# Kernel tuning notes

Measured on AMD Instinct MI355X. Metric: run time of the kernel, lower is better.

## Reference

```python
import jax, jax.numpy as jnp
import numpy as np

SIGMA = 7.0
KERNEL_SIZE = int(2 * np.ceil(SIGMA * 2) + 1)  # 29
PAD = (KERNEL_SIZE - 1) // 2  # 14


def _gaussian_kernel2d():
    variance = SIGMA ** 2
    coords = jnp.arange(KERNEL_SIZE, dtype=jnp.float32)
    mean = (KERNEL_SIZE - 1) / 2.0
    xg, yg = jnp.meshgrid(coords, coords, indexing='xy')
    k = jnp.exp(-((xg - mean) ** 2 + (yg - mean) ** 2) / (2.0 * variance))
    k = k / (2.0 * np.pi * variance)
    return k / k.sum()  # [K, K]


def setup_inputs() -> dict:
    key = jax.random.key(0)
    x = jax.random.normal(key, (8, 64, 256, 256), dtype=jnp.float32)
    return {"x": x}


def reference(x):
    channels = x.shape[1]
    k2d = _gaussian_kernel2d().astype(x.dtype)
    # depthwise weights: [C, 1, K, K] (OIHW with feature_group_count=C)
    w = jnp.broadcast_to(k2d, (channels, 1, KERNEL_SIZE, KERNEL_SIZE))
    xp = jnp.pad(x, ((0, 0), (0, 0), (PAD, PAD), (PAD, PAD)), mode='reflect')
    out = jax.lax.conv_general_dilated(
        xp, w,
        window_strides=(1, 1),
        padding='VALID',
        dimension_numbers=('NCHW', 'OIHW', 'NCHW'),
        feature_group_count=channels,
    )
    return out
```

## Files before the change

kernel.cpp:

```cpp
#include <hip/hip_runtime.h>

#define IMG   256
#define SROWS 32
#define KS    29
#define PAD   14
#define LDSS  292
#define MOFF  16

static constexpr float GK[15] = {
    1.0f,        0.98984780f, 0.96000544f, 0.91225408f, 0.84936581f,
    0.77483743f, 0.69256933f, 0.60653066f, 0.52045012f, 0.43756474f,
    0.36044779f, 0.29092381f, 0.23006630f, 0.17826398f, 0.13533528f
};
static constexpr float GSUM =
    GK[0] + 2.0f * (GK[1] + GK[2] + GK[3] + GK[4] + GK[5] + GK[6] + GK[7] +
                    GK[8] + GK[9] + GK[10] + GK[11] + GK[12] + GK[13] + GK[14]);
static constexpr float WT[29] = {
    GK[14]/GSUM, GK[13]/GSUM, GK[12]/GSUM, GK[11]/GSUM, GK[10]/GSUM, GK[9]/GSUM, GK[8]/GSUM,
    GK[7]/GSUM,  GK[6]/GSUM,  GK[5]/GSUM,  GK[4]/GSUM,  GK[3]/GSUM,  GK[2]/GSUM, GK[1]/GSUM,
    GK[0]/GSUM,
    GK[1]/GSUM,  GK[2]/GSUM,  GK[3]/GSUM,  GK[4]/GSUM,  GK[5]/GSUM,  GK[6]/GSUM, GK[7]/GSUM,
    GK[8]/GSUM,  GK[9]/GSUM,  GK[10]/GSUM, GK[11]/GSUM, GK[12]/GSUM, GK[13]/GSUM, GK[14]/GSUM
};

__device__ __forceinline__ int refl(int p) {
    int a = p < 0 ? -p : p;
    int b = 2 * (IMG - 1) - a;
    return a < b ? a : b;
}

__global__ __launch_bounds__(256, 4)
void gauss_v6(const float* __restrict__ x, float* __restrict__ out) {
    __shared__ float s[SROWS * LDSS];

    const int t   = threadIdx.x;
    const int img = blockIdx.y;
    const int y0  = blockIdx.x * SROWS;

    const float* __restrict__ src = x   + (size_t)img * (IMG * IMG);
    float*       __restrict__ dst = out + (size_t)img * (IMG * IMG);

    const int cq = t & 63;
    const int rg = t >> 6;
    const int c0 = cq * 4;

    {
        const int brow = y0 + rg * 8 - PAD;

        float4 acc[8];
        #pragma unroll
        for (int j = 0; j < 8; ++j) acc[j] = make_float4(0.f, 0.f, 0.f, 0.f);

        const bool interior = (brow >= 0) && (brow + 35 < IMG);
        if (interior) {
            const float* p = src + (size_t)brow * IMG + c0;
            #pragma unroll
            for (int ch = 0; ch < 3; ++ch) {
                float4 v[12];
                #pragma unroll
                for (int i = 0; i < 12; ++i)
                    v[i] = *(const float4*)(p + (ch * 12 + i) * IMG);
                #pragma unroll
                for (int i = 0; i < 12; ++i) {
                    const int sdx = ch * 12 + i;
                    #pragma unroll
                    for (int j = 0; j < 8; ++j) {
                        const int k = sdx - j;
                        if (k >= 0 && k < KS) {
                            acc[j].x += WT[k] * v[i].x;
                            acc[j].y += WT[k] * v[i].y;
                            acc[j].z += WT[k] * v[i].z;
                            acc[j].w += WT[k] * v[i].w;
                        }
                    }
                }
            }
        } else {
            #pragma unroll
            for (int ch = 0; ch < 3; ++ch) {
                float4 v[12];
                #pragma unroll
                for (int i = 0; i < 12; ++i)
                    v[i] = *(const float4*)(src + (size_t)refl(brow + ch * 12 + i) * IMG + c0);
                #pragma unroll
                for (int i = 0; i < 12; ++i) {
                    const int sdx = ch * 12 + i;
                    #pragma unroll
                    for (int j = 0; j < 8; ++j) {
                        const int k = sdx - j;
                        if (k >= 0 && k < KS) {
                            acc[j].x += WT[k] * v[i].x;
                            acc[j].y += WT[k] * v[i].y;
                            acc[j].z += WT[k] * v[i].z;
                            acc[j].w += WT[k] * v[i].w;
                        }
                    }
                }
            }
        }

        #pragma unroll
        for (int j = 0; j < 8; ++j)
            *(float4*)&s[(rg * 8 + j) * LDSS + MOFF + c0] = acc[j];

        if (c0 <= PAD || c0 + 3 >= IMG - 1 - PAD) {
            #pragma unroll
            for (int q = 0; q < 4; ++q) {
                const int c = c0 + q;
                if (c >= 1 && c <= PAD) {
                    #pragma unroll
                    for (int j = 0; j < 8; ++j) {
                        const float v = q == 0 ? acc[j].x : q == 1 ? acc[j].y : q == 2 ? acc[j].z : acc[j].w;
                        s[(rg * 8 + j) * LDSS + (MOFF - c)] = v;
                    }
                } else if (c >= IMG - 1 - PAD && c <= IMG - 2) {
                    #pragma unroll
                    for (int j = 0; j < 8; ++j) {
                        const float v = q == 0 ? acc[j].x : q == 1 ? acc[j].y : q == 2 ? acc[j].z : acc[j].w;
                        s[(rg * 8 + j) * LDSS + (MOFF + 2 * (IMG - 1) - c)] = v;
                    }
                }
            }
        }
    }
    __syncthreads();

    {
        #pragma unroll
        for (int r = 0; r < 8; ++r) {
            const int row = rg * 8 + r;
            const float4* w = (const float4*)&s[row * LDSS + c0];
            float4 v[9];
            #pragma unroll
            for (int m = 0; m < 9; ++m) v[m] = w[m];

            float4 o = make_float4(0.f, 0.f, 0.f, 0.f);
            #pragma unroll
            for (int m = 0; m < 9; ++m) {
                #pragma unroll
                for (int q = 0; q < 4; ++q) {
                    const int p = 4 * m + q;
                    const float val = q == 0 ? v[m].x : q == 1 ? v[m].y : q == 2 ? v[m].z : v[m].w;
                    #pragma unroll
                    for (int c = 0; c < 4; ++c) {
                        const int k = p - c - 2;
                        if (k >= 0 && k < KS) {
                            if (c == 0) o.x += WT[k] * val;
                            else if (c == 1) o.y += WT[k] * val;
                            else if (c == 2) o.z += WT[k] * val;
                            else o.w += WT[k] * val;
                        }
                    }
                }
            }
            *(float4*)&dst[(size_t)(y0 + row) * IMG + c0] = o;
        }
    }
}

extern "C" void kernel_launch(void* const* d_in, const int* in_sizes, int n_in,
                              void* d_out, int out_size, void* d_ws, size_t ws_size,
                              hipStream_t stream) {
    const float* x = (const float*)d_in[0];
    float* out = (float*)d_out;
    const int images = in_sizes[0] / (IMG * IMG);
    dim3 grid(IMG / SROWS, images);
    gauss_v6<<<grid, dim3(256), 0, stream>>>(x, out);
}
```

Before: 96.76 us.

## Halve row tile and register-block the horizontal pass at 16 outputs per thread

Each block now covers 16 output rows instead of 32. The vertical pass gives each thread 4 rows instead of 8, and launch bounds now allow 8 blocks per CU instead of 4. The horizontal pass is rewritten so that each thread produces 16 consecutive outputs of one row from 48 LDS values, instead of 4 outputs from 36 values for each of 8 rows. This cuts LDS reads per output and raises occupancy. The cost is a larger vertical halo per output row, which means more redundant global or L2 reads, and more accumulators live per thread in the horizontal pass.

```diff
diff --git a/kernel.cpp b/kernel.cpp
--- a/kernel.cpp
+++ b/kernel.cpp
@@ -1,7 +1,7 @@
 #include <hip/hip_runtime.h>
 
 #define IMG   256
-#define SROWS 32
+#define SROWS 16
 #define KS    29
 #define PAD   14
 #define LDSS  292
@@ -29,8 +29,8 @@
     return a < b ? a : b;
 }
 
-__global__ __launch_bounds__(256, 4)
-void gauss_v6(const float* __restrict__ x, float* __restrict__ out) {
+__global__ __launch_bounds__(256, 8)
+void gauss_v7(const float* __restrict__ x, float* __restrict__ out) {
     __shared__ float s[SROWS * LDSS];
 
     const int t   = threadIdx.x;
@@ -40,31 +40,30 @@
     const float* __restrict__ src = x   + (size_t)img * (IMG * IMG);
     float*       __restrict__ dst = out + (size_t)img * (IMG * IMG);
 
-    const int cq = t & 63;
-    const int rg = t >> 6;
-    const int c0 = cq * 4;
+    {
+        const int cq   = t & 63;
+        const int rg   = t >> 6;
+        const int c0   = cq * 4;
+        const int brow = y0 + rg * 4 - PAD;
 
-    {
-        const int brow = y0 + rg * 8 - PAD;
+        float4 acc[4];
+        #pragma unroll
+        for (int j = 0; j < 4; ++j) acc[j] = make_float4(0.f, 0.f, 0.f, 0.f);
 
-        float4 acc[8];
-        #pragma unroll
-        for (int j = 0; j < 8; ++j) acc[j] = make_float4(0.f, 0.f, 0.f, 0.f);
-
-        const bool interior = (brow >= 0) && (brow + 35 < IMG);
+        const bool interior = (brow >= 0) && (brow + 31 < IMG);
         if (interior) {
             const float* p = src + (size_t)brow * IMG + c0;
             #pragma unroll
-            for (int ch = 0; ch < 3; ++ch) {
-                float4 v[12];
+            for (int ch = 0; ch < 4; ++ch) {
+                float4 v[8];
                 #pragma unroll
-                for (int i = 0; i < 12; ++i)
-                    v[i] = *(const float4*)(p + (ch * 12 + i) * IMG);
+                for (int i = 0; i < 8; ++i)
+                    v[i] = *(const float4*)(p + (ch * 8 + i) * IMG);
                 #pragma unroll
-                for (int i = 0; i < 12; ++i) {
-                    const int sdx = ch * 12 + i;
+                for (int i = 0; i < 8; ++i) {
+                    const int sdx = ch * 8 + i;
                     #pragma unroll
-                    for (int j = 0; j < 8; ++j) {
+                    for (int j = 0; j < 4; ++j) {
                         const int k = sdx - j;
                         if (k >= 0 && k < KS) {
                             acc[j].x += WT[k] * v[i].x;
@@ -77,16 +76,16 @@
             }
         } else {
             #pragma unroll
-            for (int ch = 0; ch < 3; ++ch) {
-                float4 v[12];
+            for (int ch = 0; ch < 4; ++ch) {
+                float4 v[8];
                 #pragma unroll
-                for (int i = 0; i < 12; ++i)
-                    v[i] = *(const float4*)(src + (size_t)refl(brow + ch * 12 + i) * IMG + c0);
+                for (int i = 0; i < 8; ++i)
+                    v[i] = *(const float4*)(src + (size_t)refl(brow + ch * 8 + i) * IMG + c0);
                 #pragma unroll
-                for (int i = 0; i < 12; ++i) {
-                    const int sdx = ch * 12 + i;
+                for (int i = 0; i < 8; ++i) {
+                    const int sdx = ch * 8 + i;
                     #pragma unroll
-                    for (int j = 0; j < 8; ++j) {
+                    for (int j = 0; j < 4; ++j) {
                         const int k = sdx - j;
                         if (k >= 0 && k < KS) {
                             acc[j].x += WT[k] * v[i].x;
@@ -100,8 +99,8 @@
         }
 
         #pragma unroll
-        for (int j = 0; j < 8; ++j)
-            *(float4*)&s[(rg * 8 + j) * LDSS + MOFF + c0] = acc[j];
+        for (int j = 0; j < 4; ++j)
+            *(float4*)&s[(rg * 4 + j) * LDSS + MOFF + c0] = acc[j];
 
         if (c0 <= PAD || c0 + 3 >= IMG - 1 - PAD) {
             #pragma unroll
@@ -109,15 +108,15 @@
                 const int c = c0 + q;
                 if (c >= 1 && c <= PAD) {
                     #pragma unroll
-                    for (int j = 0; j < 8; ++j) {
+                    for (int j = 0; j < 4; ++j) {
                         const float v = q == 0 ? acc[j].x : q == 1 ? acc[j].y : q == 2 ? acc[j].z : acc[j].w;
-                        s[(rg * 8 + j) * LDSS + (MOFF - c)] = v;
+                        s[(rg * 4 + j) * LDSS + (MOFF - c)] = v;
                     }
                 } else if (c >= IMG - 1 - PAD && c <= IMG - 2) {
                     #pragma unroll
-                    for (int j = 0; j < 8; ++j) {
+                    for (int j = 0; j < 4; ++j) {
                         const float v = q == 0 ? acc[j].x : q == 1 ? acc[j].y : q == 2 ? acc[j].z : acc[j].w;
-                        s[(rg * 8 + j) * LDSS + (MOFF + 2 * (IMG - 1) - c)] = v;
+                        s[(rg * 4 + j) * LDSS + (MOFF + 2 * (IMG - 1) - c)] = v;
                     }
                 }
             }
@@ -126,35 +125,39 @@
     __syncthreads();
 
     {
+        const int row = t >> 4;
+        const int cg  = t & 15;
+        const int c0b = cg * 16;
+
+        float acc[16];
         #pragma unroll
-        for (int r = 0; r < 8; ++r) {
-            const int row = rg * 8 + r;
-            const float4* w = (const float4*)&s[row * LDSS + c0];
-            float4 v[9];
+        for (int c = 0; c < 16; ++c) acc[c] = 0.f;
+
+        const float4* w = (const float4*)&s[row * LDSS + c0b];
+        #pragma unroll
+        for (int ch = 0; ch < 3; ++ch) {
+            float4 v[4];
             #pragma unroll
-            for (int m = 0; m < 9; ++m) v[m] = w[m];
-
-            float4 o = make_float4(0.f, 0.f, 0.f, 0.f);
+            for (int m = 0; m < 4; ++m) v[m] = w[ch * 4 + m];
             #pragma unroll
-            for (int m = 0; m < 9; ++m) {
+            for (int m = 0; m < 4; ++m) {
                 #pragma unroll
                 for (int q = 0; q < 4; ++q) {
-                    const int p = 4 * m + q;
+                    const int e = (ch * 4 + m) * 4 + q;
                     const float val = q == 0 ? v[m].x : q == 1 ? v[m].y : q == 2 ? v[m].z : v[m].w;
                     #pragma unroll
-                    for (int c = 0; c < 4; ++c) {
-                        const int k = p - c - 2;
-                        if (k >= 0 && k < KS) {
-                            if (c == 0) o.x += WT[k] * val;
-                            else if (c == 1) o.y += WT[k] * val;
-                            else if (c == 2) o.z += WT[k] * val;
-                            else o.w += WT[k] * val;
-                        }
+                    for (int c = 0; c < 16; ++c) {
+                        const int k = e - 2 - c;
+                        if (k >= 0 && k < KS) acc[c] += WT[k] * val;
                     }
                 }
             }
-            *(float4*)&dst[(size_t)(y0 + row) * IMG + c0] = o;
         }
+
+        float4* orow = (float4*)&dst[(size_t)(y0 + row) * IMG + c0b];
+        #pragma unroll
+        for (int m = 0; m < 4; ++m)
+            orow[m] = make_float4(acc[4*m+0], acc[4*m+1], acc[4*m+2], acc[4*m+3]);
     }
 }
 
@@ -165,5 +168,5 @@
     float* out = (float*)d_out;
     const int images = in_sizes[0] / (IMG * IMG);
     dim3 grid(IMG / SROWS, images);
-    gauss_v6<<<grid, dim3(256), 0, stream>>>(x, out);
+    gauss_v7<<<grid, dim3(256), 0, stream>>>(x, out);
 }
```

Measured after the change: 204.4 us. 111% more time.
